# Optimization experiments

Measured on AMD Instinct MI355X. Metric: run time of the kernel, lower is better.

The kernel has to match this reference:

```python
import jax, jax.numpy as jnp
import numpy as np

N_NODES = 100000
N_EDGES = 1600000
D_FEAT = 128
HIDDEN = 128
NUM_LAYERS = 3
NUM_GRAPHS = 256
NUM_CLASSES = 2
TEMPERATURE = 0.5
NEGATIVE_W = 0.8


def setup_inputs() -> dict:
    key = jax.random.key(0)
    ks = jax.random.split(key, 16)
    inp = {
        "sc_x": jax.random.normal(ks[0], (N_NODES, D_FEAT), jnp.float32),
        "fc_x": jax.random.normal(ks[1], (N_NODES, D_FEAT), jnp.float32),
        "sc_edge_index": jax.random.randint(ks[2], (2, N_EDGES), 0, N_NODES, jnp.int32),
        "fc_edge_index": jax.random.randint(ks[3], (2, N_EDGES), 0, N_NODES, jnp.int32),
        "batch": jnp.sort(jax.random.randint(ks[4], (N_NODES,), 0, NUM_GRAPHS, jnp.int32)),
    }
    s = 1.0 / np.sqrt(HIDDEN)
    inp["sc_W"] = jax.random.normal(ks[5], (NUM_LAYERS, D_FEAT, HIDDEN), jnp.float32) * s
    inp["sc_b"] = jnp.zeros((NUM_LAYERS, HIDDEN), jnp.float32)
    inp["fc_W"] = jax.random.normal(ks[6], (NUM_LAYERS, D_FEAT, HIDDEN), jnp.float32) * s
    inp["fc_b"] = jnp.zeros((NUM_LAYERS, HIDDEN), jnp.float32)
    inp["fc1_W"] = jax.random.normal(ks[7], (2 * HIDDEN, HIDDEN), jnp.float32) * s
    inp["fc1_b"] = jnp.zeros((HIDDEN,), jnp.float32)
    inp["fc2_W"] = jax.random.normal(ks[8], (HIDDEN, NUM_CLASSES), jnp.float32) * s
    inp["fc2_b"] = jnp.zeros((NUM_CLASSES,), jnp.float32)
    return inp


def _gcn_branch(x, Ws, bs, edge_index):
    n = x.shape[0]
    src, dst = edge_index[0], edge_index[1]
    deg = jnp.zeros((n,), x.dtype).at[dst].add(1.0) + 1.0  # +1 for self loop
    dis = jax.lax.rsqrt(deg)
    enorm = dis[src] * dis[dst]          # [E] edge norm
    snorm = dis * dis                    # [N] self-loop norm
    for l in range(Ws.shape[0]):
        h = x @ Ws[l]                    # [N, H]
        agg = jax.ops.segment_sum(h[src] * enorm[:, None], dst, num_segments=n)
        agg = agg + h * snorm[:, None]
        x = jax.nn.relu(agg + bs[l])
    return x


def reference(sc_x, fc_x, sc_W, sc_b, fc_W, fc_b, fc1_W, fc1_b, fc2_W, fc2_b,
              sc_edge_index, fc_edge_index, batch):
    sc_h = _gcn_branch(sc_x, sc_W, sc_b, sc_edge_index)
    fc_h = _gcn_branch(fc_x, fc_W, fc_b, fc_edge_index)
    # global_add_pool -> [B, H]
    sc_g = jax.ops.segment_sum(sc_h, batch, num_segments=NUM_GRAPHS)
    fc_g = jax.ops.segment_sum(fc_h, batch, num_segments=NUM_GRAPHS)

    # classifier head (eval mode: dropout is identity)
    z = jnp.concatenate([sc_g, fc_g], axis=1)
    z = jax.nn.relu(z @ fc1_W + fc1_b)
    logp = jax.nn.log_softmax(z @ fc2_W + fc2_b, axis=-1)  # [B, C]

    # contrastive block
    B = NUM_GRAPHS
    sc_n = sc_g / jnp.maximum(jnp.linalg.norm(sc_g, axis=1, keepdims=True), 1e-12)
    fc_n = fc_g / jnp.maximum(jnp.linalg.norm(fc_g, axis=1, keepdims=True), 1e-12)
    t = 1.0 / TEMPERATURE
    logits_per_sc = (sc_n @ fc_n.T) * t
    logits_per_fc = (fc_n @ sc_n.T) * t
    off_diag = 1.0 - jnp.eye(B, dtype=sc_n.dtype)
    neg_sc = (sc_n @ sc_n.T) * t * off_diag
    neg_fc = (fc_n @ fc_n.T) * t * off_diag
    sc_logits = jnp.concatenate([logits_per_sc, NEGATIVE_W * neg_sc], axis=1)  # [B, 2B]
    fc_logits = jnp.concatenate([logits_per_fc, NEGATIVE_W * neg_fc], axis=1)
    idx = jnp.arange(B)
    loss_i = -jax.nn.log_softmax(sc_logits, axis=1)[idx, idx]
    loss_t = -jax.nn.log_softmax(fc_logits, axis=1)[idx, idx]
    return logp + (loss_i.mean() + loss_t.mean()) / 2
```

## Files before the change

### kernel.cpp

```cpp
#include <hip/hip_runtime.h>
#include <math.h>

#define N_NODES 100000
#define N_EDGES 1600000
#define HID     128
#define NGRAPH  256
#define GB      ((N_NODES + 63) / 64)
#define GAT_NB  (N_NODES / 4)
#define FGG_NB  (N_NODES / 16)
#define PB      ((N_NODES + 63) / 64)
#define NBUCK   ((N_NODES + 511) / 512)
#define AVPT    16
#define ABLK    ((N_EDGES + 256 * AVPT - 1) / (256 * AVPT))

typedef unsigned short u16;
typedef unsigned int   u32;
typedef __attribute__((ext_vector_type(8))) short    bf16x8;
typedef __attribute__((ext_vector_type(4))) float    f32x4;
typedef __attribute__((ext_vector_type(8))) unsigned short u16x8;

__device__ inline float b2f(u16 u) {
    union { unsigned int i; float f; } x; x.i = ((unsigned int)u) << 16; return x.f;
}
__device__ inline u16 f2b(float f) {
    union { float f; unsigned int i; } x; x.f = f;
    unsigned int r = x.i + 0x7fff + ((x.i >> 16) & 1);
    return (u16)(r >> 16);
}


__global__ __launch_bounds__(256) void bucket_count_kernel(
        const int* __restrict__ sc_ei, const int* __restrict__ fc_ei,
        int* __restrict__ bktcnt) {
    int b = blockIdx.x;
    int branch = b >= ABLK;
    int blk = branch ? b - ABLK : b;
    const int* dsts = (branch ? fc_ei : sc_ei) + N_EDGES;
    int* bc = bktcnt + (branch ? NBUCK : 0);
    __shared__ int hist[NBUCK];
    int tid = threadIdx.x;
    for (int i = tid; i < NBUCK; i += 256) hist[i] = 0;
    __syncthreads();
    int e0 = blk * (256 * AVPT) + tid;
    for (int k = 0; k < AVPT; ++k) {
        int e = e0 + k * 256;
        if (e < N_EDGES) atomicAdd(&hist[dsts[e] >> 9], 1);
    }
    __syncthreads();
    for (int i = tid; i < NBUCK; i += 256)
        if (hist[i]) atomicAdd(&bc[i], hist[i]);
}

__global__ __launch_bounds__(256) void bucket_scan_kernel(
        const int* __restrict__ bktcnt, int* __restrict__ bktoff, int* __restrict__ bcur) {
    __shared__ int lds[2][256];
    int tid = threadIdx.x;
    int v0 = (tid < NBUCK) ? bktcnt[tid] : 0;
    int v1 = (tid < NBUCK) ? bktcnt[NBUCK + tid] : 0;
    lds[0][tid] = v0;
    lds[1][tid] = v1;
    __syncthreads();
    for (int off = 1; off < 256; off <<= 1) {
        int t0 = (tid >= off) ? lds[0][tid - off] : 0;
        int t1 = (tid >= off) ? lds[1][tid - off] : 0;
        __syncthreads();
        lds[0][tid] += t0;
        lds[1][tid] += t1;
        __syncthreads();
    }
    if (tid < NBUCK) {
        int e0 = lds[0][tid] - v0;
        int e1 = lds[1][tid] - v1;
        bktoff[tid] = e0;
        bktoff[(NBUCK + 1) + tid] = e1;
        bcur[tid] = e0;
        bcur[NBUCK + tid] = e1;
    }
    if (tid == 0) {
        bktoff[NBUCK] = N_EDGES;
        bktoff[(NBUCK + 1) + NBUCK] = N_EDGES;
    }
}

__global__ __launch_bounds__(256) void buildA_kernel(
        const int* __restrict__ sc_ei, const int* __restrict__ fc_ei,
        int* __restrict__ bcur,
        u32* __restrict__ tmp_sc, u32* __restrict__ tmp_fc) {
    int b = blockIdx.x;
    int branch = b >= ABLK;
    int blk = branch ? b - ABLK : b;
    const int* ei = branch ? fc_ei : sc_ei;
    u32* tmp      = branch ? tmp_fc : tmp_sc;
    int* bc       = bcur + (branch ? NBUCK : 0);

    __shared__ int hist[NBUCK];
    __shared__ int cur[NBUCK];
    int tid = threadIdx.x;
    for (int i = tid; i < NBUCK; i += 256) hist[i] = 0;
    __syncthreads();

    int e0 = blk * (256 * AVPT) + tid;
    for (int k = 0; k < AVPT; ++k) {
        int e = e0 + k * 256;
        if (e < N_EDGES) atomicAdd(&hist[ei[N_EDGES + e] >> 9], 1);
    }
    __syncthreads();
    for (int i = tid; i < NBUCK; i += 256) {
        int c = hist[i];
        cur[i] = c ? atomicAdd(&bc[i], c) : 0;
    }
    __syncthreads();
    for (int k = 0; k < AVPT; ++k) {
        int e = e0 + k * 256;
        if (e < N_EDGES) {
            int s = ei[e], d = ei[N_EDGES + e];
            int pos = atomicAdd(&cur[d >> 9], 1);
            tmp[pos] = ((u32)s << 9) | (u32)(d & 511);
        }
    }
}

__global__ __launch_bounds__(256) void bucket_fin_kernel(
        const u32* __restrict__ tmp_sc, const u32* __restrict__ tmp_fc,
        const int* __restrict__ bktoff,
        int* __restrict__ off_sc, int* __restrict__ off_fc,
        float* __restrict__ d_sc, float* __restrict__ d_fc,
        int* __restrict__ srcs_sc, int* __restrict__ srcs_fc) {
    int b = blockIdx.x;
    int branch = b >= NBUCK;
    int bucket = branch ? b - NBUCK : b;
    const u32* tmp = branch ? tmp_fc : tmp_sc;
    const int* bo  = bktoff + (branch ? (NBUCK + 1) : 0);
    int* off   = branch ? off_fc : off_sc;
    float* dis = branch ? d_fc : d_sc;
    int* srcs  = branch ? srcs_fc : srcs_sc;
    int node0 = bucket << 9;
    int beg = bo[bucket], end = bo[bucket + 1];

    __shared__ int cnt[512];
    __shared__ int cur[512];
    __shared__ int psum[256];
    int tid = threadIdx.x;
    cnt[2 * tid] = 0; cnt[2 * tid + 1] = 0;
    __syncthreads();
    for (int r = beg + tid; r < end; r += 256)
        atomicAdd(&cnt[tmp[r] & 511], 1);
    __syncthreads();
    int c0 = cnt[2 * tid], c1 = cnt[2 * tid + 1];
    int s = c0 + c1;
    psum[tid] = s;
    __syncthreads();
    for (int o = 1; o < 256; o <<= 1) {
        int t = (tid >= o) ? psum[tid - o] : 0;
        __syncthreads();
        psum[tid] += t;
        __syncthreads();
    }
    int base = beg + psum[tid] - s;
    int n0 = node0 + 2 * tid, n1 = node0 + 2 * tid + 1;
    if (n0 < N_NODES) { off[n0] = base;      dis[n0] = rsqrtf((float)c0 + 1.0f); }
    if (n1 < N_NODES) { off[n1] = base + c0; dis[n1] = rsqrtf((float)c1 + 1.0f); }
    cur[2 * tid] = base;
    cur[2 * tid + 1] = base + c0;
    __syncthreads();
    for (int r = beg + tid; r < end; r += 256) {
        u32 rec = tmp[r];
        int pos = atomicAdd(&cur[rec & 511], 1);
        srcs[pos] = rec >> 9;
    }
    if (b == 0 && tid == 0) { off_sc[N_NODES] = N_EDGES; off_fc[N_NODES] = N_EDGES; }
}

__global__ void convert_w_kernel(const float* __restrict__ sc_W, const float* __restrict__ fc_W,
                                 u16* __restrict__ Wt) {
    int idx = blockIdx.x * 256 + threadIdx.x;
    if (idx >= 6 * 16384) return;
    int lp = idx >> 14;
    int r = idx & 16383;
    int n = r >> 7, k = r & 127;
    const float* W = (lp >= 3) ? fc_W : sc_W;
    int l = (lp >= 3) ? lp - 3 : lp;
    Wt[idx] = f2b(W[(size_t)l * 16384 + k * 128 + n]);
}

__global__ __launch_bounds__(256) void gemm2_kernel(
        const void* __restrict__ A_sc, const void* __restrict__ A_fc, int a_fp32,
        const u16* __restrict__ Wt, int layer,
        const float* __restrict__ d_sc, const float* __restrict__ d_fc,
        u16* __restrict__ H_sc, u16* __restrict__ H_fc) {
    int branch = blockIdx.x >= GB;
    int blk = branch ? blockIdx.x - GB : blockIdx.x;
    const void* A = branch ? A_fc : A_sc;
    const float* dis = branch ? d_fc : d_sc;
    u16* H = branch ? H_fc : H_sc;
    const u16* W = Wt + (((size_t)branch * 3 + layer) << 14);

    __shared__ u16 Alds[64 * 136];
    __shared__ u16 Wlds[128 * 136];
    const int tid = threadIdx.x;
    const int row0 = blk * 64;

    if (a_fp32) {
        const float* Af = (const float*)A;
#pragma unroll
        for (int i = 0; i < 8; ++i) {
            int idx = tid + i * 256;
            int r = idx >> 5, f = idx & 31;
            int grow = row0 + r;
            float4 v = (grow < N_NODES) ? *(const float4*)&Af[(size_t)grow * 128 + f * 4]
                                        : make_float4(0.f, 0.f, 0.f, 0.f);
            ushort4 o;
            o.x = f2b(v.x); o.y = f2b(v.y); o.z = f2b(v.z); o.w = f2b(v.w);
            *(ushort4*)&Alds[r * 136 + f * 4] = o;
        }
    } else {
        const u16* Ab = (const u16*)A;
#pragma unroll
        for (int i = 0; i < 4; ++i) {
            int idx = tid + i * 256;
            int r = idx >> 4, f = idx & 15;
            int grow = row0 + r;
            u16x8 v = {};
            if (grow < N_NODES) v = *(const u16x8*)&Ab[(size_t)grow * 128 + f * 8];
            *(u16x8*)&Alds[r * 136 + f * 8] = v;
        }
    }
#pragma unroll
    for (int i = 0; i < 8; ++i) {
        int idx = tid + i * 256;
        int n = idx >> 4, f = idx & 15;
        *(u16x8*)&Wlds[n * 136 + f * 8] = *(const u16x8*)&W[n * 128 + f * 8];
    }
    __syncthreads();

    const int wv = tid >> 6;
    const int lane = tid & 63;
    const int m = lane & 15;
    const int quad = lane >> 4;

    bf16x8 af[4];
#pragma unroll
    for (int kt = 0; kt < 4; ++kt)
        af[kt] = *(const bf16x8*)&Alds[(wv * 16 + m) * 136 + kt * 32 + quad * 8];

    f32x4 acc[8];
#pragma unroll
    for (int ct = 0; ct < 8; ++ct) { acc[ct][0] = 0.f; acc[ct][1] = 0.f; acc[ct][2] = 0.f; acc[ct][3] = 0.f; }

#pragma unroll
    for (int ct = 0; ct < 8; ++ct) {
#pragma unroll
        for (int kt = 0; kt < 4; ++kt) {
            bf16x8 bf = *(const bf16x8*)&Wlds[(ct * 16 + m) * 136 + kt * 32 + quad * 8];
            acc[ct] = __builtin_amdgcn_mfma_f32_16x16x32_bf16(af[kt], bf, acc[ct], 0, 0, 0);
        }
    }

    float4 dv = *(const float4*)&dis[row0 + wv * 16 + quad * 4];
#pragma unroll
    for (int ct = 0; ct < 8; ++ct) {
        acc[ct][0] *= dv.x; acc[ct][1] *= dv.y; acc[ct][2] *= dv.z; acc[ct][3] *= dv.w;
    }

#pragma unroll
    for (int ct = 0; ct < 8; ++ct)
#pragma unroll
        for (int r = 0; r < 4; ++r)
            Alds[(wv * 16 + quad * 4 + r) * 136 + ct * 16 + m] = f2b(acc[ct][r]);
    __syncthreads();
#pragma unroll
    for (int i = 0; i < 4; ++i) {
        int idx = i * 64 + lane;
        int r = idx >> 4, f = idx & 15;
        int grow = row0 + wv * 16 + r;
        if (grow < N_NODES)
            *(u16x8*)&H[(size_t)grow * 128 + f * 8] = *(const u16x8*)&Alds[(wv * 16 + r) * 136 + f * 8];
    }
}

__global__ __launch_bounds__(256, 6) void fgg_kernel(
        const u16* __restrict__ h_sc_in, const u16* __restrict__ h_fc_in,
        const int* __restrict__ srcs_sc, const int* __restrict__ srcs_fc,
        const int* __restrict__ off_sc, const int* __restrict__ off_fc,
        const float* __restrict__ d_sc, const float* __restrict__ d_fc,
        const float* __restrict__ b_sc, const float* __restrict__ b_fc,
        const u16* __restrict__ Wt, int wl,
        u16* __restrict__ h_sc_out, u16* __restrict__ h_fc_out) {
    int bb = blockIdx.x;
    int branch = bb >= FGG_NB;
    if (branch) bb -= FGG_NB;
    const u16* h    = branch ? h_fc_in : h_sc_in;
    const int* srcs = branch ? srcs_fc : srcs_sc;
    const int* offs = branch ? off_fc : off_sc;
    const float* dis = branch ? d_fc : d_sc;
    const float* bias = branch ? b_fc : b_sc;
    u16* hout = branch ? h_fc_out : h_sc_out;
    const u16* W = Wt + (((size_t)branch * 3 + wl) << 14);

    __shared__ u16 xt[16 * 136];

    const int tid = threadIdx.x;
    const int wv = tid >> 6;
    const int lane = tid & 63;
    const int quarter = lane >> 4;
    const int c = (lane & 15) * 8;
    const int node0 = bb * 16;

    for (int nn = 0; nn < 4; ++nn) {
        int node = node0 + wv * 4 + nn;
        int beg = offs[node], end = offs[node + 1];
        u16x8 hv = *(const u16x8*)&h[(size_t)node * 128 + c];
        float dn = dis[node];
        float acc[8] = {0.f, 0.f, 0.f, 0.f, 0.f, 0.f, 0.f, 0.f};
        for (int j = beg + quarter; j < end; j += 16) {
            int o1 = (j + 4  < end) ? 4  : 0;
            int o2 = (j + 8  < end) ? 8  : 0;
            int o3 = (j + 12 < end) ? 12 : 0;
            float m1 = o1 ? 1.f : 0.f;
            float m2 = o2 ? 1.f : 0.f;
            float m3 = o3 ? 1.f : 0.f;
            int s0 = __builtin_nontemporal_load(&srcs[j]);
            int s1 = __builtin_nontemporal_load(&srcs[j + o1]);
            int s2 = __builtin_nontemporal_load(&srcs[j + o2]);
            int s3 = __builtin_nontemporal_load(&srcs[j + o3]);
            u16x8 v0 = *(const u16x8*)&h[(size_t)s0 * 128 + c];
            u16x8 v1 = *(const u16x8*)&h[(size_t)s1 * 128 + c];
            u16x8 v2 = *(const u16x8*)&h[(size_t)s2 * 128 + c];
            u16x8 v3 = *(const u16x8*)&h[(size_t)s3 * 128 + c];
#pragma unroll
            for (int t = 0; t < 8; ++t) {
                acc[t] += b2f(v0[t]);
                acc[t] = fmaf(m1, b2f(v1[t]), acc[t]);
                acc[t] = fmaf(m2, b2f(v2[t]), acc[t]);
                acc[t] = fmaf(m3, b2f(v3[t]), acc[t]);
            }
        }
#pragma unroll
        for (int t = 0; t < 8; ++t) {
            acc[t] += __shfl_xor(acc[t], 16);
            acc[t] += __shfl_xor(acc[t], 32);
        }
        if (quarter == 0) {
            float4 b0 = *(const float4*)&bias[c];
            float4 b1 = *(const float4*)&bias[c + 4];
            float bv[8] = {b0.x, b0.y, b0.z, b0.w, b1.x, b1.y, b1.z, b1.w};
            u16x8 o;
#pragma unroll
            for (int t = 0; t < 8; ++t)
                o[t] = f2b(fmaxf(dn * (acc[t] + b2f(hv[t])) + bv[t], 0.f));
            *(u16x8*)&xt[(wv * 4 + nn) * 136 + c] = o;
        }
    }
    __syncthreads();

    const int m = lane & 15;
    const int quad = lane >> 4;
    bf16x8 af[4];
#pragma unroll
    for (int kt = 0; kt < 4; ++kt)
        af[kt] = *(const bf16x8*)&xt[m * 136 + kt * 32 + quad * 8];

    f32x4 acc2[2];
    acc2[0][0] = 0.f; acc2[0][1] = 0.f; acc2[0][2] = 0.f; acc2[0][3] = 0.f;
    acc2[1][0] = 0.f; acc2[1][1] = 0.f; acc2[1][2] = 0.f; acc2[1][3] = 0.f;
#pragma unroll
    for (int cc = 0; cc < 2; ++cc) {
        int ct = wv * 2 + cc;
        const u16* Wr = &W[(ct * 16 + m) * 128 + quad * 8];
#pragma unroll
        for (int kt = 0; kt < 4; ++kt) {
            bf16x8 bf = *(const bf16x8*)&Wr[kt * 32];
            acc2[cc] = __builtin_amdgcn_mfma_f32_16x16x32_bf16(af[kt], bf, acc2[cc], 0, 0, 0);
        }
    }
    float4 dv = *(const float4*)&dis[node0 + quad * 4];
    __syncthreads();
#pragma unroll
    for (int cc = 0; cc < 2; ++cc) {
        float dm[4] = {dv.x, dv.y, dv.z, dv.w};
#pragma unroll
        for (int r = 0; r < 4; ++r)
            xt[(quad * 4 + r) * 136 + (wv * 2 + cc) * 16 + m] = f2b(acc2[cc][r] * dm[r]);
    }
    __syncthreads();
    {
        int r = tid >> 4, f = tid & 15;
        *(u16x8*)&hout[(size_t)(node0 + r) * 128 + f * 8] = *(const u16x8*)&xt[r * 136 + f * 8];
    }
}

__global__ __launch_bounds__(256, 8) void gather2_kernel(
        const u16* __restrict__ h_sc, const u16* __restrict__ h_fc,
        const int* __restrict__ srcs_sc, const int* __restrict__ srcs_fc,
        const int* __restrict__ off_sc, const int* __restrict__ off_fc,
        const float* __restrict__ d_sc, const float* __restrict__ d_fc,
        const float* __restrict__ b_sc, const float* __restrict__ b_fc,
        u16* __restrict__ x_sc, u16* __restrict__ x_fc) {
    int bb = blockIdx.x;
    int branch = bb >= GAT_NB;
    if (branch) bb -= GAT_NB;
    const u16* h    = branch ? h_fc : h_sc;
    const int* srcs = branch ? srcs_fc : srcs_sc;
    const int* offs = branch ? off_fc : off_sc;
    const float* dis = branch ? d_fc : d_sc;
    const float* bias = branch ? b_fc : b_sc;
    u16* xout = branch ? x_fc : x_sc;

    int node = bb * 4 + (threadIdx.x >> 6);
    int lane = threadIdx.x & 63;
    int quarter = lane >> 4;
    int c = (lane & 15) * 8;
    int beg = offs[node], end = offs[node + 1];

    u16x8 hv = *(const u16x8*)&h[(size_t)node * 128 + c];
    float dn = dis[node];

    float acc[8] = {0.f, 0.f, 0.f, 0.f, 0.f, 0.f, 0.f, 0.f};
    for (int j = beg + quarter; j < end; j += 16) {
        int o1 = (j + 4  < end) ? 4  : 0;
        int o2 = (j + 8  < end) ? 8  : 0;
        int o3 = (j + 12 < end) ? 12 : 0;
        float m1 = o1 ? 1.f : 0.f;
        float m2 = o2 ? 1.f : 0.f;
        float m3 = o3 ? 1.f : 0.f;
        int s0 = __builtin_nontemporal_load(&srcs[j]);
        int s1 = __builtin_nontemporal_load(&srcs[j + o1]);
        int s2 = __builtin_nontemporal_load(&srcs[j + o2]);
        int s3 = __builtin_nontemporal_load(&srcs[j + o3]);
        u16x8 v0 = *(const u16x8*)&h[(size_t)s0 * 128 + c];
        u16x8 v1 = *(const u16x8*)&h[(size_t)s1 * 128 + c];
        u16x8 v2 = *(const u16x8*)&h[(size_t)s2 * 128 + c];
        u16x8 v3 = *(const u16x8*)&h[(size_t)s3 * 128 + c];
#pragma unroll
        for (int t = 0; t < 8; ++t) {
            acc[t] += b2f(v0[t]);
            acc[t] = fmaf(m1, b2f(v1[t]), acc[t]);
            acc[t] = fmaf(m2, b2f(v2[t]), acc[t]);
            acc[t] = fmaf(m3, b2f(v3[t]), acc[t]);
        }
    }
#pragma unroll
    for (int t = 0; t < 8; ++t) {
        acc[t] += __shfl_xor(acc[t], 16);
        acc[t] += __shfl_xor(acc[t], 32);
    }
    if (quarter == 0) {
        float4 b0 = *(const float4*)&bias[c];
        float4 b1 = *(const float4*)&bias[c + 4];
        float bv[8] = {b0.x, b0.y, b0.z, b0.w, b1.x, b1.y, b1.z, b1.w};
        u16x8 o;
#pragma unroll
        for (int t = 0; t < 8; ++t)
            o[t] = f2b(fmaxf(dn * (acc[t] + b2f(hv[t])) + bv[t], 0.f));
        __builtin_nontemporal_store(o, (u16x8*)&xout[(size_t)node * 128 + c]);
    }
}

__global__ __launch_bounds__(128) void pool2_kernel(const u16* __restrict__ x_sc,
                                                    const u16* __restrict__ x_fc,
                                                    const int* __restrict__ batch,
                                                    float* __restrict__ g_sc,
                                                    float* __restrict__ g_fc) {
    int b = blockIdx.x;
    const u16* x = (b >= PB) ? x_fc : x_sc;
    float* g     = (b >= PB) ? g_fc : g_sc;
    int blk = (b >= PB) ? b - PB : b;
    int c = threadIdx.x;
    int start = blk * 64;
    if (start >= N_NODES) return;
    int endn = min(start + 64, N_NODES);
    float acc = 0.f;
    int cur = batch[start];
    for (int i = start; i < endn; ++i) {
        int bb = batch[i];
        if (bb != cur) {
            atomicAdd(&g[(size_t)cur * 128 + c], acc);
            acc = 0.f;
            cur = bb;
        }
        acc += b2f(x[(size_t)i * 128 + c]);
    }
    atomicAdd(&g[(size_t)cur * 128 + c], acc);
}

__global__ __launch_bounds__(64) void normalize_kernel(const float* __restrict__ g_sc,
                                                       const float* __restrict__ g_fc,
                                                       float* __restrict__ n_sc,
                                                       float* __restrict__ n_fc) {
    int r = blockIdx.x & 255;
    const float* g = (blockIdx.x < 256) ? g_sc : g_fc;
    float* o = (blockIdx.x < 256) ? n_sc : n_fc;
    int c = threadIdx.x;
    float v0 = g[r * 128 + c], v1 = g[r * 128 + c + 64];
    float ss = v0 * v0 + v1 * v1;
#pragma unroll
    for (int off = 32; off; off >>= 1) ss += __shfl_xor(ss, off);
    float inv = 1.0f / fmaxf(sqrtf(ss), 1e-12f);
    o[r * 128 + c] = v0 * inv;
    o[r * 128 + c + 64] = v1 * inv;
}

__global__ __launch_bounds__(128) void head_kernel(const float* __restrict__ g_sc,
                                                   const float* __restrict__ g_fc,
                                                   const float* __restrict__ W1,
                                                   const float* __restrict__ b1,
                                                   const float* __restrict__ W2,
                                                   const float* __restrict__ b2,
                                                   float* __restrict__ out) {
    __shared__ float cat[256];
    __shared__ float red[4];
    int i = blockIdx.x, c = threadIdx.x;
    cat[c] = g_sc[i * 128 + c];
    cat[128 + c] = g_fc[i * 128 + c];
    __syncthreads();
    float acc = b1[c];
    for (int k = 0; k < 256; ++k) acc += cat[k] * W1[k * 128 + c];
    float z = fmaxf(acc, 0.f);
    float l0 = z * W2[c * 2 + 0];
    float l1 = z * W2[c * 2 + 1];
#pragma unroll
    for (int off = 32; off; off >>= 1) {
        l0 += __shfl_xor(l0, off);
        l1 += __shfl_xor(l1, off);
    }
    if ((c & 63) == 0) {
        red[(c >> 6) * 2 + 0] = l0;
        red[(c >> 6) * 2 + 1] = l1;
    }
    __syncthreads();
    if (c == 0) {
        float L0 = red[0] + red[2] + b2[0];
        float L1 = red[1] + red[3] + b2[1];
        float m = fmaxf(L0, L1);
        float lse = m + logf(expf(L0 - m) + expf(L1 - m));
        out[i * 2 + 0] = L0 - lse;
        out[i * 2 + 1] = L1 - lse;
    }
}

__global__ __launch_bounds__(256) void contrast_kernel(const float* __restrict__ n_sc,
                                                       const float* __restrict__ n_fc,
                                                       float* __restrict__ loss_acc) {
    __shared__ float arow[128];
    __shared__ float redm[4];
    __shared__ float reds[4];
    __shared__ float diag_s;
    int b = blockIdx.x;
    int i = b & 255;
    bool which = b >= 256;
    const float* A  = which ? n_fc : n_sc;
    const float* B1 = which ? n_sc : n_fc;
    const float* B2 = which ? n_fc : n_sc;
    int j = threadIdx.x;
    if (j < 128) arow[j] = A[i * 128 + j];
    __syncthreads();
    float d1 = 0.f, d2 = 0.f;
    for (int k = 0; k < 128; ++k) {
        float a = arow[k];
        d1 += a * B1[(size_t)j * 128 + k];
        d2 += a * B2[(size_t)j * 128 + k];
    }
    const float t = 2.0f;
    float v1 = t * d1;
    float v2 = (j == i) ? 0.0f : 0.8f * t * d2;
    if (j == i) diag_s = v1;
    float m = fmaxf(v1, v2);
#pragma unroll
    for (int off = 32; off; off >>= 1) m = fmaxf(m, __shfl_xor(m, off));
    if ((j & 63) == 0) redm[j >> 6] = m;
    __syncthreads();
    m = fmaxf(fmaxf(redm[0], redm[1]), fmaxf(redm[2], redm[3]));
    float s = expf(v1 - m) + expf(v2 - m);
#pragma unroll
    for (int off = 32; off; off >>= 1) s += __shfl_xor(s, off);
    if ((j & 63) == 0) reds[j >> 6] = s;
    __syncthreads();
    if (j == 0) {
        float S = reds[0] + reds[1] + reds[2] + reds[3];
        float lse = m + logf(S);
        atomicAdd(loss_acc, lse - diag_s);
    }
}

__global__ void final_add(float* __restrict__ out, const float* __restrict__ loss) {
    int t = threadIdx.x;
    if (t < 512) out[t] += loss[0] * (1.0f / 512.0f);
}


extern "C" void kernel_launch(void* const* d_in, const int* in_sizes, int n_in,
                              void* d_out, int out_size, void* d_ws, size_t ws_size,
                              hipStream_t stream) {
    const float* sc_x  = (const float*)d_in[0];
    const float* fc_x  = (const float*)d_in[1];
    const int*   sc_ei = (const int*)d_in[2];
    const int*   fc_ei = (const int*)d_in[3];
    const int*   batch = (const int*)d_in[4];
    const float* sc_W  = (const float*)d_in[5];
    const float* sc_b  = (const float*)d_in[6];
    const float* fc_W  = (const float*)d_in[7];
    const float* fc_b  = (const float*)d_in[8];
    const float* fc1_W = (const float*)d_in[9];
    const float* fc1_b = (const float*)d_in[10];
    const float* fc2_W = (const float*)d_in[11];
    const float* fc2_b = (const float*)d_in[12];
    float* out = (float*)d_out;

    const size_t NF = (size_t)N_NODES * HID;

    float* ws = (float*)d_ws;
    float* dis_sc = ws;
    float* dis_fc = dis_sc + N_NODES;
    float* g_sc  = dis_fc + N_NODES;
    float* g_fc  = g_sc + NGRAPH * HID;
    float* n_sc  = g_fc + NGRAPH * HID;
    float* n_fc  = n_sc + NGRAPH * HID;
    float* lossp = n_fc + NGRAPH * HID;
    u16* h_sc    = (u16*)(lossp + 4);
    u16* h_fc    = h_sc + NF;
    u16* x_sc    = h_fc + NF;
    u16* x_fc    = x_sc + NF;
    u16* Wtb     = x_fc + NF;
    int* srcs_sc   = (int*)(Wtb + 6 * 16384);
    int* srcs_fc   = srcs_sc + N_EDGES;
    u32* tmp_sc    = (u32*)(srcs_fc + N_EDGES);
    u32* tmp_fc    = tmp_sc + N_EDGES;
    int* off_sc    = (int*)(tmp_fc + N_EDGES);
    int* off_fc    = off_sc + (N_NODES + 1);
    int* bcur      = off_fc + (N_NODES + 1);
    int* bktcnt    = bcur + 2 * NBUCK;
    int* bktoff    = bktcnt + 2 * NBUCK;
    (void)ws_size; (void)n_in; (void)in_sizes; (void)out_size;

    hipMemsetAsync(bktcnt, 0, 2 * NBUCK * sizeof(int), stream);
    bucket_count_kernel<<<2 * ABLK, 256, 0, stream>>>(sc_ei, fc_ei, bktcnt);
    bucket_scan_kernel<<<1, 256, 0, stream>>>(bktcnt, bktoff, bcur);
    buildA_kernel<<<2 * ABLK, 256, 0, stream>>>(sc_ei, fc_ei, bcur, tmp_sc, tmp_fc);
    bucket_fin_kernel<<<2 * NBUCK, 256, 0, stream>>>(tmp_sc, tmp_fc, bktoff,
                                                     off_sc, off_fc, dis_sc, dis_fc,
                                                     srcs_sc, srcs_fc);
    convert_w_kernel<<<(6 * 16384 + 255) / 256, 256, 0, stream>>>(sc_W, fc_W, Wtb);

    gemm2_kernel<<<2 * GB, 256, 0, stream>>>(sc_x, fc_x, 1, Wtb, 0,
                                             dis_sc, dis_fc, h_sc, h_fc);
    fgg_kernel<<<2 * FGG_NB, 256, 0, stream>>>(
        h_sc, h_fc, srcs_sc, srcs_fc, off_sc, off_fc, dis_sc, dis_fc,
        sc_b, fc_b, Wtb, 1, x_sc, x_fc);
    fgg_kernel<<<2 * FGG_NB, 256, 0, stream>>>(
        x_sc, x_fc, srcs_sc, srcs_fc, off_sc, off_fc, dis_sc, dis_fc,
        sc_b + HID, fc_b + HID, Wtb, 2, h_sc, h_fc);
    gather2_kernel<<<2 * GAT_NB, 256, 0, stream>>>(
        h_sc, h_fc, srcs_sc, srcs_fc, off_sc, off_fc,
        dis_sc, dis_fc, sc_b + 2 * HID, fc_b + 2 * HID, x_sc, x_fc);

    hipMemsetAsync(g_sc, 0, 2 * NGRAPH * HID * sizeof(float), stream);
    pool2_kernel<<<2 * PB, 128, 0, stream>>>(x_sc, x_fc, batch, g_sc, g_fc);

    normalize_kernel<<<512, 64, 0, stream>>>(g_sc, g_fc, n_sc, n_fc);
    head_kernel<<<NGRAPH, 128, 0, stream>>>(g_sc, g_fc, fc1_W, fc1_b, fc2_W, fc2_b, out);
    hipMemsetAsync(lossp, 0, sizeof(float), stream);
    contrast_kernel<<<512, 256, 0, stream>>>(n_sc, n_fc, lossp);
    final_add<<<1, 512, 0, stream>>>(out, lossp);
}
```

Baseline: 882.8 us.

## Replace bucket count pass with fixed-capacity arenas and split per-branch gather launches

Drops the separate bucket counting kernel and its scan by giving each destination bucket a fixed-capacity arena (BCAP slots) in the temporary buffer. A small scan after scatter derives the final CSR offsets. buildA now keeps the edge src/dst values in registers between the histogram and scatter phases instead of reloading them. The combined two-branch fgg/gather launches are split into separate per-branch launches, which makes the kernel signatures simpler and may improve cache locality per branch. This relies on no bucket exceeding BCAP edges, which holds for uniform random inputs but would overflow on skewed graphs.

```diff
diff --git a/kernel.cpp b/kernel.cpp
--- a/kernel.cpp
+++ b/kernel.cpp
@@ -10,6 +10,7 @@
 #define FGG_NB  (N_NODES / 16)
 #define PB      ((N_NODES + 63) / 64)
 #define NBUCK   ((N_NODES + 511) / 512)
+#define BCAP    12288
 #define AVPT    16
 #define ABLK    ((N_EDGES + 256 * AVPT - 1) / (256 * AVPT))
 
@@ -29,57 +30,11 @@
 }
 
 
-__global__ __launch_bounds__(256) void bucket_count_kernel(
-        const int* __restrict__ sc_ei, const int* __restrict__ fc_ei,
-        int* __restrict__ bktcnt) {
-    int b = blockIdx.x;
-    int branch = b >= ABLK;
-    int blk = branch ? b - ABLK : b;
-    const int* dsts = (branch ? fc_ei : sc_ei) + N_EDGES;
-    int* bc = bktcnt + (branch ? NBUCK : 0);
-    __shared__ int hist[NBUCK];
-    int tid = threadIdx.x;
-    for (int i = tid; i < NBUCK; i += 256) hist[i] = 0;
-    __syncthreads();
-    int e0 = blk * (256 * AVPT) + tid;
-    for (int k = 0; k < AVPT; ++k) {
-        int e = e0 + k * 256;
-        if (e < N_EDGES) atomicAdd(&hist[dsts[e] >> 9], 1);
-    }
-    __syncthreads();
-    for (int i = tid; i < NBUCK; i += 256)
-        if (hist[i]) atomicAdd(&bc[i], hist[i]);
-}
-
-__global__ __launch_bounds__(256) void bucket_scan_kernel(
-        const int* __restrict__ bktcnt, int* __restrict__ bktoff, int* __restrict__ bcur) {
-    __shared__ int lds[2][256];
-    int tid = threadIdx.x;
-    int v0 = (tid < NBUCK) ? bktcnt[tid] : 0;
-    int v1 = (tid < NBUCK) ? bktcnt[NBUCK + tid] : 0;
-    lds[0][tid] = v0;
-    lds[1][tid] = v1;
-    __syncthreads();
-    for (int off = 1; off < 256; off <<= 1) {
-        int t0 = (tid >= off) ? lds[0][tid - off] : 0;
-        int t1 = (tid >= off) ? lds[1][tid - off] : 0;
-        __syncthreads();
-        lds[0][tid] += t0;
-        lds[1][tid] += t1;
-        __syncthreads();
-    }
-    if (tid < NBUCK) {
-        int e0 = lds[0][tid] - v0;
-        int e1 = lds[1][tid] - v1;
-        bktoff[tid] = e0;
-        bktoff[(NBUCK + 1) + tid] = e1;
-        bcur[tid] = e0;
-        bcur[NBUCK + tid] = e1;
-    }
-    if (tid == 0) {
-        bktoff[NBUCK] = N_EDGES;
-        bktoff[(NBUCK + 1) + NBUCK] = N_EDGES;
-    }
+__global__ void bcur_init_kernel(int* __restrict__ bcur) {
+    int t = threadIdx.x;
+    if (t >= 2 * NBUCK) return;
+    int k = (t >= NBUCK) ? t - NBUCK : t;
+    bcur[t] = k * BCAP;
 }
 
 __global__ __launch_bounds__(256) void buildA_kernel(
@@ -100,9 +55,14 @@
     __syncthreads();
 
     int e0 = blk * (256 * AVPT) + tid;
+    int ss[AVPT], dd[AVPT];
+#pragma unroll
     for (int k = 0; k < AVPT; ++k) {
         int e = e0 + k * 256;
-        if (e < N_EDGES) atomicAdd(&hist[ei[N_EDGES + e] >> 9], 1);
+        bool v = e < N_EDGES;
+        ss[k] = v ? ei[e] : 0;
+        dd[k] = v ? ei[N_EDGES + e] : -1;
+        if (v) atomicAdd(&hist[dd[k] >> 9], 1);
     }
     __syncthreads();
     for (int i = tid; i < NBUCK; i += 256) {
@@ -110,19 +70,45 @@
         cur[i] = c ? atomicAdd(&bc[i], c) : 0;
     }
     __syncthreads();
+#pragma unroll
     for (int k = 0; k < AVPT; ++k) {
-        int e = e0 + k * 256;
-        if (e < N_EDGES) {
-            int s = ei[e], d = ei[N_EDGES + e];
-            int pos = atomicAdd(&cur[d >> 9], 1);
-            tmp[pos] = ((u32)s << 9) | (u32)(d & 511);
-        }
+        if (dd[k] >= 0) {
+            int pos = atomicAdd(&cur[dd[k] >> 9], 1);
+            tmp[pos] = ((u32)ss[k] << 9) | (u32)(dd[k] & 511);
+        }
+    }
+}
+
+__global__ __launch_bounds__(256) void arena_scan_kernel(
+        const int* __restrict__ bcur, int* __restrict__ bktoff) {
+    __shared__ int lds[2][256];
+    int tid = threadIdx.x;
+    int v0 = (tid < NBUCK) ? bcur[tid] - tid * BCAP : 0;
+    int v1 = (tid < NBUCK) ? bcur[NBUCK + tid] - tid * BCAP : 0;
+    lds[0][tid] = v0;
+    lds[1][tid] = v1;
+    __syncthreads();
+    for (int off = 1; off < 256; off <<= 1) {
+        int t0 = (tid >= off) ? lds[0][tid - off] : 0;
+        int t1 = (tid >= off) ? lds[1][tid - off] : 0;
+        __syncthreads();
+        lds[0][tid] += t0;
+        lds[1][tid] += t1;
+        __syncthreads();
+    }
+    if (tid < NBUCK) {
+        bktoff[tid] = lds[0][tid] - v0;
+        bktoff[(NBUCK + 1) + tid] = lds[1][tid] - v1;
+    }
+    if (tid == 0) {
+        bktoff[NBUCK] = N_EDGES;
+        bktoff[(NBUCK + 1) + NBUCK] = N_EDGES;
     }
 }
 
 __global__ __launch_bounds__(256) void bucket_fin_kernel(
         const u32* __restrict__ tmp_sc, const u32* __restrict__ tmp_fc,
-        const int* __restrict__ bktoff,
+        const int* __restrict__ bcur, const int* __restrict__ bktoff,
         int* __restrict__ off_sc, int* __restrict__ off_fc,
         float* __restrict__ d_sc, float* __restrict__ d_fc,
         int* __restrict__ srcs_sc, int* __restrict__ srcs_fc) {
@@ -135,7 +121,9 @@
     float* dis = branch ? d_fc : d_sc;
     int* srcs  = branch ? srcs_fc : srcs_sc;
     int node0 = bucket << 9;
-    int beg = bo[bucket], end = bo[bucket + 1];
+    int beg_t = bucket * BCAP;
+    int end_t = bcur[branch * NBUCK + bucket];
+    int csr0  = bo[bucket];
 
     __shared__ int cnt[512];
     __shared__ int cur[512];
@@ -143,7 +131,7 @@
     int tid = threadIdx.x;
     cnt[2 * tid] = 0; cnt[2 * tid + 1] = 0;
     __syncthreads();
-    for (int r = beg + tid; r < end; r += 256)
+    for (int r = beg_t + tid; r < end_t; r += 256)
         atomicAdd(&cnt[tmp[r] & 511], 1);
     __syncthreads();
     int c0 = cnt[2 * tid], c1 = cnt[2 * tid + 1];
@@ -156,14 +144,14 @@
         psum[tid] += t;
         __syncthreads();
     }
-    int base = beg + psum[tid] - s;
+    int base = csr0 + psum[tid] - s;
     int n0 = node0 + 2 * tid, n1 = node0 + 2 * tid + 1;
     if (n0 < N_NODES) { off[n0] = base;      dis[n0] = rsqrtf((float)c0 + 1.0f); }
     if (n1 < N_NODES) { off[n1] = base + c0; dis[n1] = rsqrtf((float)c1 + 1.0f); }
     cur[2 * tid] = base;
     cur[2 * tid + 1] = base + c0;
     __syncthreads();
-    for (int r = beg + tid; r < end; r += 256) {
+    for (int r = beg_t + tid; r < end_t; r += 256) {
         u32 rec = tmp[r];
         int pos = atomicAdd(&cur[rec & 511], 1);
         srcs[pos] = rec >> 9;
@@ -279,24 +267,12 @@
 }
 
 __global__ __launch_bounds__(256, 6) void fgg_kernel(
-        const u16* __restrict__ h_sc_in, const u16* __restrict__ h_fc_in,
-        const int* __restrict__ srcs_sc, const int* __restrict__ srcs_fc,
-        const int* __restrict__ off_sc, const int* __restrict__ off_fc,
-        const float* __restrict__ d_sc, const float* __restrict__ d_fc,
-        const float* __restrict__ b_sc, const float* __restrict__ b_fc,
-        const u16* __restrict__ Wt, int wl,
-        u16* __restrict__ h_sc_out, u16* __restrict__ h_fc_out) {
+        const u16* __restrict__ h, const int* __restrict__ srcs,
+        const int* __restrict__ offs, const float* __restrict__ dis,
+        const float* __restrict__ bias,
+        const u16* __restrict__ W,
+        u16* __restrict__ hout) {
     int bb = blockIdx.x;
-    int branch = bb >= FGG_NB;
-    if (branch) bb -= FGG_NB;
-    const u16* h    = branch ? h_fc_in : h_sc_in;
-    const int* srcs = branch ? srcs_fc : srcs_sc;
-    const int* offs = branch ? off_fc : off_sc;
-    const float* dis = branch ? d_fc : d_sc;
-    const float* bias = branch ? b_fc : b_sc;
-    u16* hout = branch ? h_fc_out : h_sc_out;
-    const u16* W = Wt + (((size_t)branch * 3 + wl) << 14);
-
     __shared__ u16 xt[16 * 136];
 
     const int tid = threadIdx.x;
@@ -390,22 +366,10 @@
 }
 
 __global__ __launch_bounds__(256, 8) void gather2_kernel(
-        const u16* __restrict__ h_sc, const u16* __restrict__ h_fc,
-        const int* __restrict__ srcs_sc, const int* __restrict__ srcs_fc,
-        const int* __restrict__ off_sc, const int* __restrict__ off_fc,
-        const float* __restrict__ d_sc, const float* __restrict__ d_fc,
-        const float* __restrict__ b_sc, const float* __restrict__ b_fc,
-        u16* __restrict__ x_sc, u16* __restrict__ x_fc) {
+        const u16* __restrict__ h, const int* __restrict__ srcs,
+        const int* __restrict__ offs, const float* __restrict__ dis,
+        const float* __restrict__ bias, u16* __restrict__ xout) {
     int bb = blockIdx.x;
-    int branch = bb >= GAT_NB;
-    if (branch) bb -= GAT_NB;
-    const u16* h    = branch ? h_fc : h_sc;
-    const int* srcs = branch ? srcs_fc : srcs_sc;
-    const int* offs = branch ? off_fc : off_sc;
-    const float* dis = branch ? d_fc : d_sc;
-    const float* bias = branch ? b_fc : b_sc;
-    u16* xout = branch ? x_fc : x_sc;
-
     int node = bb * 4 + (threadIdx.x >> 6);
     int lane = threadIdx.x & 63;
     int quarter = lane >> 4;
@@ -607,6 +571,7 @@
     float* out = (float*)d_out;
 
     const size_t NF = (size_t)N_NODES * HID;
+    const size_t TMPSZ = (size_t)NBUCK * BCAP;
 
     float* ws = (float*)d_ws;
     float* dis_sc = ws;
@@ -624,34 +589,35 @@
     int* srcs_sc   = (int*)(Wtb + 6 * 16384);
     int* srcs_fc   = srcs_sc + N_EDGES;
     u32* tmp_sc    = (u32*)(srcs_fc + N_EDGES);
-    u32* tmp_fc    = tmp_sc + N_EDGES;
-    int* off_sc    = (int*)(tmp_fc + N_EDGES);
+    u32* tmp_fc    = tmp_sc + TMPSZ;
+    int* off_sc    = (int*)(tmp_fc + TMPSZ);
     int* off_fc    = off_sc + (N_NODES + 1);
     int* bcur      = off_fc + (N_NODES + 1);
-    int* bktcnt    = bcur + 2 * NBUCK;
-    int* bktoff    = bktcnt + 2 * NBUCK;
+    int* bktoff    = bcur + 2 * NBUCK;
     (void)ws_size; (void)n_in; (void)in_sizes; (void)out_size;
 
-    hipMemsetAsync(bktcnt, 0, 2 * NBUCK * sizeof(int), stream);
-    bucket_count_kernel<<<2 * ABLK, 256, 0, stream>>>(sc_ei, fc_ei, bktcnt);
-    bucket_scan_kernel<<<1, 256, 0, stream>>>(bktcnt, bktoff, bcur);
+    bcur_init_kernel<<<1, 512, 0, stream>>>(bcur);
     buildA_kernel<<<2 * ABLK, 256, 0, stream>>>(sc_ei, fc_ei, bcur, tmp_sc, tmp_fc);
-    bucket_fin_kernel<<<2 * NBUCK, 256, 0, stream>>>(tmp_sc, tmp_fc, bktoff,
+    arena_scan_kernel<<<1, 256, 0, stream>>>(bcur, bktoff);
+    bucket_fin_kernel<<<2 * NBUCK, 256, 0, stream>>>(tmp_sc, tmp_fc, bcur, bktoff,
                                                      off_sc, off_fc, dis_sc, dis_fc,
                                                      srcs_sc, srcs_fc);
     convert_w_kernel<<<(6 * 16384 + 255) / 256, 256, 0, stream>>>(sc_W, fc_W, Wtb);
 
     gemm2_kernel<<<2 * GB, 256, 0, stream>>>(sc_x, fc_x, 1, Wtb, 0,
                                              dis_sc, dis_fc, h_sc, h_fc);
-    fgg_kernel<<<2 * FGG_NB, 256, 0, stream>>>(
-        h_sc, h_fc, srcs_sc, srcs_fc, off_sc, off_fc, dis_sc, dis_fc,
-        sc_b, fc_b, Wtb, 1, x_sc, x_fc);
-    fgg_kernel<<<2 * FGG_NB, 256, 0, stream>>>(
-        x_sc, x_fc, srcs_sc, srcs_fc, off_sc, off_fc, dis_sc, dis_fc,
-        sc_b + HID, fc_b + HID, Wtb, 2, h_sc, h_fc);
-    gather2_kernel<<<2 * GAT_NB, 256, 0, stream>>>(
-        h_sc, h_fc, srcs_sc, srcs_fc, off_sc, off_fc,
-        dis_sc, dis_fc, sc_b + 2 * HID, fc_b + 2 * HID, x_sc, x_fc);
+    fgg_kernel<<<FGG_NB, 256, 0, stream>>>(h_sc, srcs_sc, off_sc, dis_sc,
+                                           sc_b, Wtb + ((size_t)1 << 14), x_sc);
+    fgg_kernel<<<FGG_NB, 256, 0, stream>>>(h_fc, srcs_fc, off_fc, dis_fc,
+                                           fc_b, Wtb + ((size_t)4 << 14), x_fc);
+    fgg_kernel<<<FGG_NB, 256, 0, stream>>>(x_sc, srcs_sc, off_sc, dis_sc,
+                                           sc_b + HID, Wtb + ((size_t)2 << 14), h_sc);
+    fgg_kernel<<<FGG_NB, 256, 0, stream>>>(x_fc, srcs_fc, off_fc, dis_fc,
+                                           fc_b + HID, Wtb + ((size_t)5 << 14), h_fc);
+    gather2_kernel<<<GAT_NB, 256, 0, stream>>>(h_sc, srcs_sc, off_sc, dis_sc,
+                                               sc_b + 2 * HID, x_sc);
+    gather2_kernel<<<GAT_NB, 256, 0, stream>>>(h_fc, srcs_fc, off_fc, dis_fc,
+                                               fc_b + 2 * HID, x_fc);
 
     hipMemsetAsync(g_sc, 0, 2 * NGRAPH * HID * sizeof(float), stream);
     pool2_kernel<<<2 * PB, 128, 0, stream>>>(x_sc, x_fc, batch, g_sc, g_fc);
```

Measured after the change: 872.8 us. Within noise of the previous version (-1.1%).
